# Kernel optimization log

Measured on AMD Instinct MI355X. Metric: run time of the kernel, lower is better.

The kernel has to match this reference:

```python
import jax, jax.numpy as jnp
import numpy as np

TEMP = 0.5  # RelaxedBernoulli temperature
EPS = 1e-6


def setup_inputs() -> dict:
    B, T, D = 8, 2048, 512
    key = jax.random.key(0)
    kx, ku, k1, k2 = jax.random.split(key, 4)
    x = jax.random.normal(kx, (B, T, D), dtype=jnp.float32)
    u = jax.random.uniform(ku, (B, T), dtype=jnp.float32, minval=EPS, maxval=1.0 - EPS)
    # upstream linear initialized to identity (per module __init__)
    W_up = jnp.eye(D, dtype=jnp.float32)
    s = 1.0 / np.sqrt(D)
    W1 = jax.random.normal(k1, (D, D), dtype=jnp.float32) * s
    b1 = jnp.zeros((D,), dtype=jnp.float32)
    W2 = jax.random.normal(k2, (1, D), dtype=jnp.float32) * s
    b2 = jnp.zeros((1,), dtype=jnp.float32)  # init_bias = 0.0
    return {"x": x, "u": u, "W_up": W_up, "W1": W1, "b1": b1, "W2": W2, "b2": b2}


def reference(x, u, W_up, W1, b1, W2, b2):
    B, T, D = x.shape
    # upstream linear (no bias); torch Linear computes x @ W^T
    hidden = jnp.einsum('btd,ed->bte', x, W_up)
    # boundary MLP: Linear -> GELU(exact) -> Linear(out=1), then sigmoid
    h = jax.nn.gelu(jnp.einsum('btd,ed->bte', hidden, W1) + b1, approximate=False)
    logits = jnp.einsum('btd,od->bto', h, W2)[..., 0] + b2[0]  # [B,T]
    probs = jax.nn.sigmoid(logits)
    # RelaxedBernoulli rsample with explicit uniform noise u (straight-through hard)
    p = jnp.clip(probs, EPS, 1.0 - EPS)
    uu = jnp.clip(u, EPS, 1.0 - EPS)
    soft = jax.nn.sigmoid((jnp.log(p) - jnp.log1p(-p) + jnp.log(uu) - jnp.log1p(-uu)) / TEMP)
    hard = jax.lax.stop_gradient((soft > 0.5).astype(x.dtype))
    boundaries = hard + soft - jax.lax.stop_gradient(soft)
    # guarantee at least one boundary per row (set last frame to 1.0)
    row_sum = jnp.sum(jax.lax.stop_gradient(boundaries), axis=1)
    boundaries = boundaries.at[:, -1].set(jnp.where(row_sum == 0, 1.0, boundaries[:, -1]))
    # mean pooling over segments; segments padded to S = T (static upper bound)
    S = T
    seg_id = jnp.cumsum(boundaries, axis=1) - boundaries  # hh1 in original, [B,T]
    foo = jnp.arange(S, dtype=x.dtype)[None, None, :] - seg_id[:, :, None]  # [B,T,S]
    in_seg = jax.lax.stop_gradient(foo) == 0
    soft_mask = jnp.where(in_seg, 1.0 - foo, 0.0)  # value 1 where in segment, grad -d(foo)
    counts = jnp.clip(jnp.sum(soft_mask, axis=1), 1e-8, None)  # [B,S]
    seg_sum = jnp.einsum('bts,btd->bsd', soft_mask, hidden)  # bmm mean-pool
    pooled = seg_sum / counts[:, :, None]  # rows past true n_segments are zero
    return pooled, boundaries, probs, hidden
```

## Files before the change

### kernel.cpp

```cpp
#include <hip/hip_runtime.h>
#include <cstdint>
#include <cstddef>

typedef _Float16 half8 __attribute__((ext_vector_type(8)));
typedef float floatx4 __attribute__((ext_vector_type(4)));

constexpr int Bc = 8, Tc = 2048, Dc = 512;
constexpr float kSplitScale = 2048.0f;
constexpr float kInvSplit   = 4.8828125e-4f;
constexpr float kF16MinNorm = 6.103515625e-5f;

__device__ __forceinline__ void split8(const float* __restrict__ in, _Float16* __restrict__ hi,
                                       _Float16* __restrict__ lo, int i)
{
    const float4* ip = reinterpret_cast<const float4*>(in) + 2 * i;
    float4 a = ip[0], b = ip[1];
    float v[8] = {a.x, a.y, a.z, a.w, b.x, b.y, b.z, b.w};
    half8 h, l;
#pragma unroll
    for (int e = 0; e < 8; ++e) {
        float hv = (fabsf(v[e]) >= kF16MinNorm) ? (float)(_Float16)v[e] : 0.0f;
        h[e] = (_Float16)hv;
        l[e] = (_Float16)((v[e] - hv) * kSplitScale);
    }
    reinterpret_cast<half8*>(hi)[i] = h;
    reinterpret_cast<half8*>(lo)[i] = l;
}

__global__ __launch_bounds__(256)
void split_kernel(const float* __restrict__ in, _Float16* __restrict__ hi,
                  _Float16* __restrict__ lo, int n8)
{
    int i = blockIdx.x * 256 + threadIdx.x;
    if (i >= n8) return;
    split8(in, hi, lo, i);
}

__global__ __launch_bounds__(256)
void split3_kernel(const float* __restrict__ x,  _Float16* __restrict__ xh,  _Float16* __restrict__ xl,  int nx8,
                   const float* __restrict__ wu, _Float16* __restrict__ wuh, _Float16* __restrict__ wul, int nw8,
                   const float* __restrict__ w1, _Float16* __restrict__ w1h, _Float16* __restrict__ w1l)
{
    int i = blockIdx.x * 256 + threadIdx.x;
    if (i < nx8) { split8(x, xh, xl, i); return; }
    i -= nx8;
    if (i < nw8) { split8(wu, wuh, wul, i); return; }
    i -= nw8;
    if (i < nw8) { split8(w1, w1h, w1l, i); return; }
}

template<bool LOGITS>
__global__ __launch_bounds__(256)
void mfma_gemm(const _Float16* __restrict__ Ah, const _Float16* __restrict__ Al,
               const _Float16* __restrict__ Bh, const _Float16* __restrict__ Bl,
               float* __restrict__ C, const float* __restrict__ bias,
               const float* __restrict__ w2, float* __restrict__ logits,
               int M, int N, int K)
{
    __shared__ _Float16 As[128 * 64];
    __shared__ _Float16 Bs[128 * 64];
    const int t = threadIdx.x;
    const int bm = blockIdx.x * 128;
    const int bn = blockIdx.y * 128;
    const int lane = t & 63;
    const int wid = t >> 6;
    const int wr = (wid >> 1) * 64;
    const int wc = (wid & 1) * 64;
    const int rr = lane >> 3;
    const int ss = lane & 7;
    const int gchunk = (ss ^ rr) * 8;

    floatx4 acc[4][4];
#pragma unroll
    for (int i = 0; i < 4; ++i)
#pragma unroll
        for (int j = 0; j < 4; ++j) acc[i][j] = floatx4{0.f, 0.f, 0.f, 0.f};

    for (int c = 0; c < 3; ++c) {
        const _Float16* Asrc = (c == 1) ? Al : Ah;
        const _Float16* Bsrc = (c == 0) ? Bl : Bh;
        for (int k0 = 0; k0 < K; k0 += 64) {
            __syncthreads();
#pragma unroll
            for (int i = 0; i < 4; ++i) {
                const int rbase = i * 32 + wid * 8;
                __builtin_amdgcn_global_load_lds(
                    (const __attribute__((address_space(1))) void*)
                        (Asrc + (size_t)(bm + rbase + rr) * K + k0 + gchunk),
                    (__attribute__((address_space(3))) void*)(As + rbase * 64),
                    16, 0, 0);
                __builtin_amdgcn_global_load_lds(
                    (const __attribute__((address_space(1))) void*)
                        (Bsrc + (size_t)(bn + rbase + rr) * K + k0 + gchunk),
                    (__attribute__((address_space(3))) void*)(Bs + rbase * 64),
                    16, 0, 0);
            }
            __syncthreads();
#pragma unroll
            for (int kk = 0; kk < 2; ++kk) {
                half8 af[4], bf[4];
                const int kb = kk * 64 + ((lane >> 4) * 16);
#pragma unroll
                for (int i = 0; i < 4; ++i) {
                    const int rowa = wr + i * 16 + (lane & 15);
                    af[i] = *reinterpret_cast<const half8*>(
                        reinterpret_cast<const char*>(As) + rowa * 128 + (kb ^ ((rowa & 7) * 16)));
                    const int rowb = wc + i * 16 + (lane & 15);
                    bf[i] = *reinterpret_cast<const half8*>(
                        reinterpret_cast<const char*>(Bs) + rowb * 128 + (kb ^ ((rowb & 7) * 16)));
                }
#pragma unroll
                for (int i = 0; i < 4; ++i)
#pragma unroll
                    for (int j = 0; j < 4; ++j)
                        acc[i][j] = __builtin_amdgcn_mfma_f32_16x16x32_f16(af[i], bf[j], acc[i][j], 0, 0, 0);
            }
        }
        if (c == 1) {
#pragma unroll
            for (int i = 0; i < 4; ++i)
#pragma unroll
                for (int j = 0; j < 4; ++j)
#pragma unroll
                    for (int r = 0; r < 4; ++r) acc[i][j][r] *= kInvSplit;
        }
    }

    if (!LOGITS) {
#pragma unroll
        for (int i = 0; i < 4; ++i) {
            const int m = bm + wr + i * 16 + ((lane >> 4) * 4);
#pragma unroll
            for (int j = 0; j < 4; ++j) {
                const int n = bn + wc + j * 16 + (lane & 15);
#pragma unroll
                for (int r = 0; r < 4; ++r)
                    C[(size_t)(m + r) * N + n] = acc[i][j][r];
            }
        }
    } else {
        float b1v[4], w2v[4];
#pragma unroll
        for (int j = 0; j < 4; ++j) {
            const int n = bn + wc + j * 16 + (lane & 15);
            b1v[j] = bias[n];
            w2v[j] = w2[n];
        }
#pragma unroll
        for (int i = 0; i < 4; ++i) {
            float part[4] = {0.f, 0.f, 0.f, 0.f};
#pragma unroll
            for (int j = 0; j < 4; ++j)
#pragma unroll
                for (int r = 0; r < 4; ++r) {
                    const float v = acc[i][j][r] + b1v[j];
                    const float g = 0.5f * v * (1.0f + erff(v * 0.70710678118654752f));
                    part[r] += g * w2v[j];
                }
#pragma unroll
            for (int r = 0; r < 4; ++r) {
                float p = part[r];
                p += __shfl_xor(p, 1);
                p += __shfl_xor(p, 2);
                p += __shfl_xor(p, 4);
                p += __shfl_xor(p, 8);
                if ((lane & 15) == 0) {
                    const int m = bm + wr + i * 16 + ((lane >> 4) * 4) + r;
                    atomicAdd(&logits[m], p);
                }
            }
        }
    }
}

__global__ __launch_bounds__(256)
void probs_bnd_kernel(const float* __restrict__ logits, const float* __restrict__ b2,
                      const float* __restrict__ u, float* __restrict__ probs,
                      float* __restrict__ bnd, int n)
{
    int i = blockIdx.x * 256 + threadIdx.x;
    if (i >= n) return;
    const float lg = logits[i] + b2[0];
    const float p = 1.0f / (1.0f + expf(-lg));
    probs[i] = p;
    const float pc = fminf(fmaxf(p, 1e-6f), 1.0f - 1e-6f);
    const float uu = fminf(fmaxf(u[i], 1e-6f), 1.0f - 1e-6f);
    const float z = (logf(pc) - log1pf(-pc) + logf(uu) - log1pf(-uu)) * 2.0f;
    bnd[i] = (z > 0.0f) ? 1.0f : 0.0f;
}

__global__ __launch_bounds__(64)
void scan_fix(float* __restrict__ bnd, int* __restrict__ starts, float* __restrict__ counts)
{
    __shared__ float cnt[Tc];
    const int b = blockIdx.x;
    const int lane = threadIdx.x;
    constexpr int CH = Tc / 64;
    float* rb = bnd + (size_t)b * Tc;
    float v[CH];
    int lsum = 0;
#pragma unroll
    for (int j = 0; j < CH; ++j) { v[j] = rb[lane * CH + j]; lsum += (v[j] > 0.5f); }
    int tot = lsum;
#pragma unroll
    for (int off = 32; off >= 1; off >>= 1) tot += __shfl_xor(tot, off);
    const float prevLast = __shfl_up(v[CH - 1], 1);
    if (tot == 0 && lane == 63) { v[CH - 1] = 1.0f; rb[Tc - 1] = 1.0f; }
    int incl = lsum;
#pragma unroll
    for (int off = 1; off < 64; off <<= 1) {
        const int nv = __shfl_up(incl, off);
        if (lane >= off) incl += nv;
    }
    int run = incl - lsum;
    for (int s = lane; s < Tc; s += 64) cnt[s] = 0.0f;
    __syncthreads();
    float prev = (lane == 0) ? 1.0f : prevLast;
#pragma unroll
    for (int j = 0; j < CH; ++j) {
        const int t_ = lane * CH + j;
        if (prev > 0.5f) starts[(size_t)b * Tc + run] = t_;
        atomicAdd(&cnt[run], 1.0f);
        run += (v[j] > 0.5f);
        prev = v[j];
    }
    __syncthreads();
    for (int s = lane; s < Tc; s += 64) counts[(size_t)b * Tc + s] = cnt[s];
}

__global__ __launch_bounds__(128)
void pool_kernel(const float* __restrict__ hidden, const int* __restrict__ starts,
                 const float* __restrict__ counts, float* __restrict__ pooled)
{
    const int blk = blockIdx.x;
    const int b = blk >> 11;
    float4* outp = reinterpret_cast<float4*>(pooled + (size_t)blk * Dc) + threadIdx.x;
    const float c = counts[blk];
    if (c < 0.5f) { *outp = float4{0.f, 0.f, 0.f, 0.f}; return; }
    const int len = (int)c;
    const int start = starts[blk];
    const float4* hp = reinterpret_cast<const float4*>(
                           hidden + ((size_t)(b << 11) + start) * Dc) + threadIdx.x;
    double s0 = 0, s1 = 0, s2 = 0, s3 = 0;
    for (int r = 0; r < len; ++r) {
        const float4 v = hp[(size_t)r * (Dc / 4)];
        s0 += v.x; s1 += v.y; s2 += v.z; s3 += v.w;
    }
    const double inv = 1.0 / (double)len;
    *outp = float4{(float)(s0 * inv), (float)(s1 * inv), (float)(s2 * inv), (float)(s3 * inv)};
}

extern "C" void kernel_launch(void* const* d_in, const int* in_sizes, int n_in,
                              void* d_out, int out_size, void* d_ws, size_t ws_size,
                              hipStream_t stream)
{
    const float* x   = (const float*)d_in[0];
    const float* u   = (const float*)d_in[1];
    const float* Wup = (const float*)d_in[2];
    const float* W1  = (const float*)d_in[3];
    const float* b1  = (const float*)d_in[4];
    const float* W2  = (const float*)d_in[5];
    const float* b2  = (const float*)d_in[6];

    float* out = (float*)d_out;
    const size_t MT = (size_t)Bc * Tc;
    const size_t pooledN = MT * Dc;
    float* pooled = out;
    float* bnd    = out + pooledN;
    float* probs  = bnd + MT;
    float* hidden = probs + MT;

    _Float16* xh = (_Float16*)pooled;
    _Float16* xl = xh + pooledN;
    _Float16* hh = xh;
    _Float16* hl = xl;

    char* ws = (char*)d_ws;
    _Float16* wuh = (_Float16*)ws;  ws += (size_t)Dc * Dc * 2;
    _Float16* wul = (_Float16*)ws;  ws += (size_t)Dc * Dc * 2;
    _Float16* w1h = (_Float16*)ws;  ws += (size_t)Dc * Dc * 2;
    _Float16* w1l = (_Float16*)ws;  ws += (size_t)Dc * Dc * 2;
    float* logits = (float*)ws;     ws += MT * 4;
    int*   starts = (int*)ws;       ws += MT * 4;
    float* counts = (float*)ws;     ws += MT * 4;

    const int M = (int)MT, N = Dc, K = Dc;
    const int nx8 = M * K / 8;
    const int nw8 = K * K / 8;

    split3_kernel<<<(nx8 + 2 * nw8 + 255) / 256, 256, 0, stream>>>(
        x, xh, xl, nx8, Wup, wuh, wul, nw8, W1, w1h, w1l);

    dim3 gg(M / 128, N / 128);
    mfma_gemm<false><<<gg, 256, 0, stream>>>(xh, xl, wuh, wul, hidden,
                                             nullptr, nullptr, nullptr, M, N, K);
    split_kernel<<<(nx8 + 255) / 256, 256, 0, stream>>>(hidden, hh, hl, nx8);
    hipMemsetAsync(logits, 0, MT * 4, stream);
    mfma_gemm<true><<<gg, 256, 0, stream>>>(hh, hl, w1h, w1l, nullptr,
                                            b1, W2, logits, M, N, K);
    probs_bnd_kernel<<<((int)MT + 255) / 256, 256, 0, stream>>>(logits, b2, u, probs, bnd, (int)MT);
    scan_fix<<<Bc, 64, 0, stream>>>(bnd, starts, counts);
    pool_kernel<<<(int)MT, 128, 0, stream>>>(hidden, starts, counts, pooled);
}
```

Before: 204.5 us.

## Double-buffer LDS tiles to overlap global loads with MFMA compute

Splits the GEMM tiles into two LDS buffers and flattens the split-precision and K loops into a single 24-stage loop. The next stage's global-to-LDS load is issued before computing on the current buffer, with one barrier per stage instead of two. This hides global load latency behind MFMA work, at the cost of doubling LDS use, which may lower occupancy. It also hardcodes K=512, since there are 8 stages per component.

```diff
diff --git a/kernel.cpp b/kernel.cpp
--- a/kernel.cpp
+++ b/kernel.cpp
@@ -57,8 +57,8 @@
                const float* __restrict__ w2, float* __restrict__ logits,
                int M, int N, int K)
 {
-    __shared__ _Float16 As[128 * 64];
-    __shared__ _Float16 Bs[128 * 64];
+    __shared__ _Float16 As[2][128 * 64];
+    __shared__ _Float16 Bs[2][128 * 64];
     const int t = threadIdx.x;
     const int bm = blockIdx.x * 128;
     const int bn = blockIdx.y * 128;
@@ -76,54 +76,63 @@
 #pragma unroll
         for (int j = 0; j < 4; ++j) acc[i][j] = floatx4{0.f, 0.f, 0.f, 0.f};
 
-    for (int c = 0; c < 3; ++c) {
+    auto stage = [&](int st) {
+        const int c  = st >> 3;
+        const int k0 = (st & 7) << 6;
         const _Float16* Asrc = (c == 1) ? Al : Ah;
         const _Float16* Bsrc = (c == 0) ? Bl : Bh;
-        for (int k0 = 0; k0 < K; k0 += 64) {
-            __syncthreads();
+        _Float16* Ad = As[st & 1];
+        _Float16* Bd = Bs[st & 1];
+#pragma unroll
+        for (int i = 0; i < 4; ++i) {
+            const int rbase = i * 32 + wid * 8;
+            __builtin_amdgcn_global_load_lds(
+                (const __attribute__((address_space(1))) void*)
+                    (Asrc + (size_t)(bm + rbase + rr) * K + k0 + gchunk),
+                (__attribute__((address_space(3))) void*)(Ad + rbase * 64),
+                16, 0, 0);
+            __builtin_amdgcn_global_load_lds(
+                (const __attribute__((address_space(1))) void*)
+                    (Bsrc + (size_t)(bn + rbase + rr) * K + k0 + gchunk),
+                (__attribute__((address_space(3))) void*)(Bd + rbase * 64),
+                16, 0, 0);
+        }
+    };
+
+    stage(0);
+    __syncthreads();
+
+#pragma unroll 2
+    for (int st = 0; st < 24; ++st) {
+        if (st < 23) stage(st + 1);
+        const char* Ab = reinterpret_cast<const char*>(As[st & 1]);
+        const char* Bb = reinterpret_cast<const char*>(Bs[st & 1]);
+#pragma unroll
+        for (int kk = 0; kk < 2; ++kk) {
+            half8 af[4], bf[4];
+            const int kb = kk * 64 + ((lane >> 4) * 16);
 #pragma unroll
             for (int i = 0; i < 4; ++i) {
-                const int rbase = i * 32 + wid * 8;
-                __builtin_amdgcn_global_load_lds(
-                    (const __attribute__((address_space(1))) void*)
-                        (Asrc + (size_t)(bm + rbase + rr) * K + k0 + gchunk),
-                    (__attribute__((address_space(3))) void*)(As + rbase * 64),
-                    16, 0, 0);
-                __builtin_amdgcn_global_load_lds(
-                    (const __attribute__((address_space(1))) void*)
-                        (Bsrc + (size_t)(bn + rbase + rr) * K + k0 + gchunk),
-                    (__attribute__((address_space(3))) void*)(Bs + rbase * 64),
-                    16, 0, 0);
+                const int rowa = wr + i * 16 + (lane & 15);
+                af[i] = *reinterpret_cast<const half8*>(Ab + rowa * 128 + (kb ^ ((rowa & 7) * 16)));
+                const int rowb = wc + i * 16 + (lane & 15);
+                bf[i] = *reinterpret_cast<const half8*>(Bb + rowb * 128 + (kb ^ ((rowb & 7) * 16)));
             }
-            __syncthreads();
-#pragma unroll
-            for (int kk = 0; kk < 2; ++kk) {
-                half8 af[4], bf[4];
-                const int kb = kk * 64 + ((lane >> 4) * 16);
-#pragma unroll
-                for (int i = 0; i < 4; ++i) {
-                    const int rowa = wr + i * 16 + (lane & 15);
-                    af[i] = *reinterpret_cast<const half8*>(
-                        reinterpret_cast<const char*>(As) + rowa * 128 + (kb ^ ((rowa & 7) * 16)));
-                    const int rowb = wc + i * 16 + (lane & 15);
-                    bf[i] = *reinterpret_cast<const half8*>(
-                        reinterpret_cast<const char*>(Bs) + rowb * 128 + (kb ^ ((rowb & 7) * 16)));
-                }
-#pragma unroll
-                for (int i = 0; i < 4; ++i)
-#pragma unroll
-                    for (int j = 0; j < 4; ++j)
-                        acc[i][j] = __builtin_amdgcn_mfma_f32_16x16x32_f16(af[i], bf[j], acc[i][j], 0, 0, 0);
-            }
-        }
-        if (c == 1) {
 #pragma unroll
             for (int i = 0; i < 4; ++i)
 #pragma unroll
                 for (int j = 0; j < 4; ++j)
+                    acc[i][j] = __builtin_amdgcn_mfma_f32_16x16x32_f16(af[i], bf[j], acc[i][j], 0, 0, 0);
+        }
+        if (st == 15) {
+#pragma unroll
+            for (int i = 0; i < 4; ++i)
+#pragma unroll
+                for (int j = 0; j < 4; ++j)
 #pragma unroll
                     for (int r = 0; r < 4; ++r) acc[i][j][r] *= kInvSplit;
         }
+        __syncthreads();
     }
 
     if (!LOGITS) {
```

Result: no change. 202.1 us (-1.1%).
